# Kernel optimization log

Measured on AMD Instinct MI355X. Metric: run time of the kernel, lower is better.

## Reference

```python
import jax, jax.numpy as jnp
import numpy as np

EPSILON = 1e-4  # self.epsilon


def setup_inputs() -> dict:
    key = jax.random.key(0)
    ks = jax.random.split(key, 7)
    N, C_in, L = 32, 128, 512
    C_p, P, n_cls = 64, 2000, 200
    x = jax.random.normal(ks[0], (N, C_in, L), dtype=jnp.float32)
    W1 = jax.random.normal(ks[1], (C_p, C_in, 1), dtype=jnp.float32) * 0.05
    b1 = jnp.zeros((C_p,), dtype=jnp.float32)
    W2 = jax.random.normal(ks[2], (C_p, C_p, 1), dtype=jnp.float32) * 0.05
    b2 = jnp.zeros((C_p,), dtype=jnp.float32)
    prototype_vectors = jax.random.uniform(ks[3], (P, C_p, 1), dtype=jnp.float32)
    last_w = jax.random.normal(ks[4], (n_cls, P), dtype=jnp.float32) * 0.02
    return {"x": x, "W1": W1, "b1": b1, "W2": W2, "b2": b2,
            "prototype_vectors": prototype_vectors, "last_w": last_w}


def _forward(x, W1, b1, W2, b2, prototype_vectors, last_w):
    # add_on_layers: 1x1 conv1d -> relu -> 1x1 conv1d -> sigmoid
    h = jax.nn.relu(jnp.einsum('ncl,oc->nol', x, W1[:, :, 0]) + b1[None, :, None])
    f = jax.nn.sigmoid(jnp.einsum('ncl,oc->nol', h, W2[:, :, 0]) + b2[None, :, None])
    # _l2_convolution (prototype kernel length 1, stride 1):
    # x2_patch_sum via conv with all-ones filter == per-position channel sum of f^2
    x2_patch_sum = jnp.sum(f * f, axis=1, keepdims=True)          # [N,1,L]
    p2 = jnp.sum(prototype_vectors ** 2, axis=(1, 2))             # [P]
    xp = jnp.einsum('ncl,pc->npl', f, prototype_vectors[:, :, 0])  # [N,P,L]
    distances = jax.nn.relu(x2_patch_sum - 2.0 * xp + p2[None, :, None])
    # -max_pool(-d) over full length == min over L
    min_distances = jnp.min(distances, axis=2)                    # [N,P]
    prototype_activations = jnp.log((min_distances + 1.0) / (min_distances + EPSILON))
    logits = prototype_activations @ last_w.T                     # [N,num_classes]
    return logits, min_distances


def reference(x, W1, b1, W2, b2, prototype_vectors, last_w):
    return _forward(x, W1, b1, W2, b2, prototype_vectors, last_w)
```

## Files before the change

### kernel.cpp

```cpp
#include <hip/hip_runtime.h>
#include <hip/hip_fp16.h>
#include <math.h>

#define EPS 1e-4f
#define N_   32
#define CIN  128
#define L_   512
#define CP   64
#define P_   2000
#define NCLS 200

typedef __attribute__((ext_vector_type(8))) _Float16 f16x8;
typedef __attribute__((ext_vector_type(4))) float f32x4;

__device__ inline void gl_lds16(const void* g, void* l) {
    __builtin_amdgcn_global_load_lds(
        (const __attribute__((address_space(1))) unsigned int*)g,
        (__attribute__((address_space(3))) unsigned int*)l, 16, 0, 0);
}
__device__ inline unsigned int packh2(float a, float b) {
    unsigned int lo = __half_as_ushort(__float2half(a));
    unsigned int hi = __half_as_ushort(__float2half(b));
    return lo | (hi << 16);
}
__device__ inline unsigned short f2bf_rne(float f) {
    unsigned int u = __float_as_uint(f);
    unsigned int r = u + 0x7FFFu + ((u >> 16) & 1u);
    return (unsigned short)(r >> 16);
}
__device__ inline float bfdot2(unsigned a, unsigned b, float acc) {
    float a0 = __uint_as_float(a << 16);
    float a1 = __uint_as_float(a & 0xFFFF0000u);
    float b0 = __uint_as_float(b << 16);
    float b1 = __uint_as_float(b & 0xFFFF0000u);
    return fmaf(a1, b1, fmaf(a0, b0, acc));
}

__global__ __launch_bounds__(256) void k0_proto(const float* __restrict__ proto,
    const float* __restrict__ W1, const float* __restrict__ W2,
    const float* __restrict__ last_w,
    unsigned short* __restrict__ ph, unsigned short* __restrict__ w1h,
    unsigned short* __restrict__ w2h, unsigned short* __restrict__ lwB,
    float* __restrict__ p2)
{
    const int tid = threadIdx.x;
    const int bx  = blockIdx.x;
    if (bx >= 502) {
        int idx8 = (bx - 502)*256 + tid;
        if (idx8 < 50000) {
            const float4* src = (const float4*)(last_w + (size_t)idx8*8);
            float4 v0 = src[0], v1 = src[1];
            unsigned short o[8] = { f2bf_rne(v0.x), f2bf_rne(v0.y), f2bf_rne(v0.z), f2bf_rne(v0.w),
                                    f2bf_rne(v1.x), f2bf_rne(v1.y), f2bf_rne(v1.z), f2bf_rne(v1.w) };
            *(uint4*)(lwB + (size_t)idx8*8) = *(const uint4*)o;
        }
        return;
    }
    if (bx == 500) {
        #pragma unroll
        for (int i = 0; i < 32; ++i) {
            int idx = i*256 + tid;
            w1h[idx] = __half_as_ushort(__float2half(W1[idx]));
        }
        return;
    }
    if (bx == 501) {
        #pragma unroll
        for (int i = 0; i < 16; ++i) {
            int idx = i*256 + tid;
            w2h[idx] = __half_as_ushort(__float2half(W2[idx]));
        }
        return;
    }
    const int p = bx*4 + (tid >> 6);
    const int k = tid & 63;
    float v = proto[(size_t)p*64 + k];
    ph[(size_t)p*64 + k] = __half_as_ushort(__float2half(v));
    float s = v*v;
    #pragma unroll
    for (int off = 32; off > 0; off >>= 1) s += __shfl_xor(s, off);
    if (k == 0) p2[p] = s;
}

__global__ __launch_bounds__(256) void k1_conv(const float* __restrict__ x,
    const unsigned short* __restrict__ w1h, const float* __restrict__ b1,
    const unsigned short* __restrict__ w2h, const float* __restrict__ b2,
    unsigned short* __restrict__ fT, float* __restrict__ x2buf)
{
    __shared__ float xS[128*32];
    __shared__ __align__(16) unsigned short hb[32*72];
    __shared__ float x2p[2][32];

    const int tid  = threadIdx.x;
    const int lane = tid & 63;
    const int wv   = tid >> 6;
    const int n    = blockIdx.y;
    const int lg   = blockIdx.x;

    {
        const float* xbase = x + (size_t)n*CIN*L_ + lg*32;
        #pragma unroll
        for (int i = 0; i < 4; ++i) {
            int blk = wv*4 + i;
            const float* src = xbase + (size_t)(blk*8 + (lane >> 3))*L_ + (lane & 7)*4;
            gl_lds16(src, &xS[blk*256]);
        }
    }
    __syncthreads();

    const int r  = lane & 15;
    const int g  = lane >> 4;
    const int lt = wv & 1;
    const int oh = wv >> 1;
    const int lrow = lt*16 + r;

    f32x4 acc[2];
    #pragma unroll
    for (int o2 = 0; o2 < 2; ++o2)
        acc[o2] = *(const f32x4*)(b1 + (oh*2 + o2)*16 + g*4);

    #pragma unroll
    for (int ks = 0; ks < 4; ++ks) {
        f16x8 B;
        #pragma unroll
        for (int i = 0; i < 8; ++i)
            B[i] = (_Float16)xS[(ks*32 + g*8 + i)*32 + lrow];
        #pragma unroll
        for (int o2 = 0; o2 < 2; ++o2) {
            int ot = oh*2 + o2;
            f16x8 A = *(const f16x8*)(w1h + (ot*16 + r)*128 + ks*32 + g*8);
            acc[o2] = __builtin_amdgcn_mfma_f32_16x16x32_f16(A, B, acc[o2], 0, 0, 0);
        }
    }
    #pragma unroll
    for (int o2 = 0; o2 < 2; ++o2) {
        int ot = oh*2 + o2;
        float v0 = fmaxf(acc[o2][0], 0.f), v1 = fmaxf(acc[o2][1], 0.f);
        float v2 = fmaxf(acc[o2][2], 0.f), v3 = fmaxf(acc[o2][3], 0.f);
        uint2 w2v = make_uint2(packh2(v0, v1), packh2(v2, v3));
        *(uint2*)((char*)hb + lrow*144 + ot*32 + g*8) = w2v;
    }
    __syncthreads();

    f32x4 acc2[2];
    #pragma unroll
    for (int o2 = 0; o2 < 2; ++o2)
        acc2[o2] = *(const f32x4*)(b2 + (oh*2 + o2)*16 + g*4);

    #pragma unroll
    for (int ks = 0; ks < 2; ++ks) {
        f16x8 B = *(const f16x8*)((const char*)hb + lrow*144 + ks*64 + g*16);
        #pragma unroll
        for (int o2 = 0; o2 < 2; ++o2) {
            int ot = oh*2 + o2;
            f16x8 A = *(const f16x8*)(w2h + (ot*16 + r)*64 + ks*32 + g*8);
            acc2[o2] = __builtin_amdgcn_mfma_f32_16x16x32_f16(A, B, acc2[o2], 0, 0, 0);
        }
    }

    char* gb = (char*)xS;
    float s = 0.f;
    float fv[2][4];
    #pragma unroll
    for (int o2 = 0; o2 < 2; ++o2)
        #pragma unroll
        for (int j = 0; j < 4; ++j) {
            float v = 1.f/(1.f + expf(-acc2[o2][j]));
            fv[o2][j] = v;
            s = fmaf(v, v, s);
        }
    s += __shfl_xor(s, 16);
    s += __shfl_xor(s, 32);
    if (lane < 16) x2p[oh][lrow] = s;

    #pragma unroll
    for (int o2 = 0; o2 < 2; ++o2) {
        int ot = oh*2 + o2;
        uint2 w2v = make_uint2(packh2(fv[o2][0], fv[o2][1]), packh2(fv[o2][2], fv[o2][3]));
        *(uint2*)(gb + lrow*144 + ot*32 + g*8) = w2v;
    }
    __syncthreads();

    {
        int l = tid >> 3, u = tid & 7;
        uint4 v = *(const uint4*)(gb + l*144 + u*16);
        ((uint4*)fT)[((size_t)(n*L_ + lg*32 + l))*8 + u] = v;
    }
    if (tid < 32)
        x2buf[n*L_ + lg*32 + tid] = x2p[0][tid] + x2p[1][tid];
}

__global__ __launch_bounds__(256) void k2_dist(
    const unsigned short* __restrict__ fT, const unsigned short* __restrict__ ph,
    const float* __restrict__ x2buf, float* __restrict__ md_part)
{
    __shared__ unsigned short fB[4096];
    __shared__ float x2S[64];

    const int tid  = threadIdx.x;
    const int lane = tid & 63;
    const int wv   = tid >> 6;
    const int n    = blockIdx.y;
    const int lg   = blockIdx.x >> 2;
    const int pg   = blockIdx.x & 3;

    {
        const char* gH = (const char*)(fT + ((size_t)n*L_ + lg*64)*CP);
        #pragma unroll
        for (int j = 0; j < 2; ++j) {
            int d  = tid*32 + j*16;
            int lr = d >> 7;
            int bo = d & 127;
            int pb = (lr << 7) + (bo ^ ((lr & 7) << 4));
            *(uint4*)((char*)fB + pb) = *(const uint4*)(gH + d);
        }
    }
    if (tid < 64) x2S[tid] = x2buf[n*L_ + lg*64 + tid];
    __syncthreads();

    const int g  = lane >> 4;
    const int pr = lane & 15;

    f16x8 af[4][2];
    #pragma unroll
    for (int lt = 0; lt < 4; ++lt) {
        int lrow = lt*16 + pr;
        #pragma unroll
        for (int ks = 0; ks < 2; ++ks) {
            int bo = (ks*64 + g*16) ^ ((lrow & 7) << 4);
            af[lt][ks] = *(const f16x8*)((const char*)fB + lrow*128 + bo);
        }
    }
    float4 xv[4];
    #pragma unroll
    for (int lt = 0; lt < 4; ++lt)
        xv[lt] = *(const float4*)&x2S[lt*16 + g*4];

    float* mp = md_part + ((size_t)lg*N_ + n)*P_;

    const int t0 = pg + 4*wv;
    f16x8 bA[2], bB[2], bC[2];
    {
        const int p = t0*16 + pr;
        #pragma unroll
        for (int ks = 0; ks < 2; ++ks)
            bA[ks] = *(const f16x8*)(ph + (size_t)p*64 + ks*32 + g*8);
    }
    if (t0 + 16 < P_/16) {
        const int p = (t0+16)*16 + pr;
        #pragma unroll
        for (int ks = 0; ks < 2; ++ks)
            bB[ks] = *(const f16x8*)(ph + (size_t)p*64 + ks*32 + g*8);
    }
    for (int t = t0; t < P_/16; t += 16) {
        const int t2 = t + 32;
        if (t2 < P_/16) {
            const int p = t2*16 + pr;
            #pragma unroll
            for (int ks = 0; ks < 2; ++ks)
                bC[ks] = *(const f16x8*)(ph + (size_t)p*64 + ks*32 + g*8);
        }

        float cm0 = 3.0e38f, cm1 = 3.0e38f, cm2 = 3.0e38f, cm3 = 3.0e38f;
        #pragma unroll
        for (int lt = 0; lt < 4; ++lt) {
            f32x4 c = {0.f, 0.f, 0.f, 0.f};
            c = __builtin_amdgcn_mfma_f32_16x16x32_f16(af[lt][0], bA[0], c, 0, 0, 0);
            c = __builtin_amdgcn_mfma_f32_16x16x32_f16(af[lt][1], bA[1], c, 0, 0, 0);
            cm0 = fminf(cm0, fmaf(-2.f, c[0], xv[lt].x));
            cm1 = fminf(cm1, fmaf(-2.f, c[1], xv[lt].y));
            cm2 = fminf(cm2, fmaf(-2.f, c[2], xv[lt].z));
            cm3 = fminf(cm3, fmaf(-2.f, c[3], xv[lt].w));
        }
        float v = fminf(fminf(cm0, cm1), fminf(cm2, cm3));
        v = fminf(v, __shfl_xor(v, 16));
        v = fminf(v, __shfl_xor(v, 32));
        if (lane < 16) mp[t*16 + lane] = v;

        bA[0] = bB[0]; bA[1] = bB[1];
        bB[0] = bC[0]; bB[1] = bC[1];
    }
}

__global__ __launch_bounds__(256) void k2b_reduce(const float* __restrict__ md_part,
    const float* __restrict__ p2, float* __restrict__ md_out,
    unsigned short* __restrict__ actsB)
{
    const int p = blockIdx.x*256 + threadIdx.x;
    const int n = blockIdx.y;
    if (p < P_) {
        float mv = 3.0e38f;
        #pragma unroll
        for (int lg = 0; lg < 8; ++lg)
            mv = fminf(mv, md_part[((size_t)lg*N_ + n)*P_ + p]);
        float m = fmaxf(mv + p2[p], 0.0f);
        md_out[n*P_ + p] = m;
        actsB[(size_t)n*P_ + p] = f2bf_rne(logf((m + 1.0f) / (m + EPS)));
    }
}

__global__ __launch_bounds__(256) void k3_logits(const unsigned short* __restrict__ actsB,
    const unsigned short* __restrict__ lwB, float* __restrict__ out)
{
    const int wid  = (blockIdx.x * 256 + threadIdx.x) >> 6;
    const int lane = threadIdx.x & 63;
    const int n    = wid / NCLS;
    const int cls  = wid - n * NCLS;

    const uint4* a = (const uint4*)(actsB + (size_t)n*P_);
    const uint4* w = (const uint4*)(lwB + (size_t)cls*P_);

    float acc = 0.f;
    #pragma unroll
    for (int it = 0; it < 4; ++it) {
        int idx = it*64 + lane;
        if (idx < P_/8) {
            uint4 av = a[idx], wv = w[idx];
            acc = bfdot2(av.x, wv.x, acc);
            acc = bfdot2(av.y, wv.y, acc);
            acc = bfdot2(av.z, wv.z, acc);
            acc = bfdot2(av.w, wv.w, acc);
        }
    }
    #pragma unroll
    for (int off = 32; off > 0; off >>= 1)
        acc += __shfl_down(acc, off);
    if (lane == 0)
        out[n*NCLS + cls] = acc;
}

extern "C" void kernel_launch(void* const* d_in, const int* in_sizes, int n_in,
                              void* d_out, int out_size, void* d_ws, size_t ws_size,
                              hipStream_t stream)
{
    const float* x      = (const float*)d_in[0];
    const float* W1     = (const float*)d_in[1];
    const float* b1     = (const float*)d_in[2];
    const float* W2     = (const float*)d_in[3];
    const float* b2     = (const float*)d_in[4];
    const float* proto  = (const float*)d_in[5];
    const float* last_w = (const float*)d_in[6];

    float* out = (float*)d_out;

    unsigned short* fT = (unsigned short*)d_ws;
    float* x2buf = (float*)(fT + (size_t)N_*L_*CP);
    unsigned short* actsB = (unsigned short*)(x2buf + (size_t)N_*L_);
    unsigned short* ph = actsB + (size_t)N_*P_;
    float* p2      = (float*)(ph + (size_t)P_*CP);
    float* md_part = p2 + P_;
    unsigned short* w1h = (unsigned short*)(md_part + (size_t)8*N_*P_);
    unsigned short* w2h = w1h + 64*CIN;
    unsigned short* lwB = w2h + 64*CP;

    k0_proto  <<<698,           256, 0, stream>>>(proto, W1, W2, last_w,
                                                  ph, w1h, w2h, lwB, p2);
    k1_conv   <<<dim3(16, 32),  256, 0, stream>>>(x, w1h, b1, w2h, b2, fT, x2buf);
    k2_dist   <<<dim3(32, 32),  256, 0, stream>>>(fT, ph, x2buf, md_part);
    k2b_reduce<<<dim3(8, 32),   256, 0, stream>>>(md_part, p2, out + N_*NCLS, actsB);
    k3_logits <<<1600,          256, 0, stream>>>(actsB, lwB, out);
}
```

Before: 35.17 us.

## Fuse weight prep into conv kernel and reduce into logits kernel

Merges the prototype/weight conversion kernel into the conv kernel as extra blocks. W1/W2 are now converted to fp16 inline from fp32 global memory instead of through a separate precomputed buffer. Also fuses the min-reduction and activation computation with the logits GEMV, keeping activations in shared memory, so the launch count drops from five to three. In exchange, each of the 8 class-group blocks per sample recomputes the full reduction, and W1/W2 conversion work is repeated in every conv block.

```diff
diff --git a/kernel.cpp b/kernel.cpp
--- a/kernel.cpp
+++ b/kernel.cpp
@@ -35,67 +35,57 @@
     float b1 = __uint_as_float(b & 0xFFFF0000u);
     return fmaf(a1, b1, fmaf(a0, b0, acc));
 }
-
-__global__ __launch_bounds__(256) void k0_proto(const float* __restrict__ proto,
-    const float* __restrict__ W1, const float* __restrict__ W2,
-    const float* __restrict__ last_w,
-    unsigned short* __restrict__ ph, unsigned short* __restrict__ w1h,
-    unsigned short* __restrict__ w2h, unsigned short* __restrict__ lwB,
+__device__ inline f16x8 cvt8(const float* p) {
+    float4 a0 = *(const float4*)p, a1 = *(const float4*)(p + 4);
+    f16x8 r;
+    r[0]=(_Float16)a0.x; r[1]=(_Float16)a0.y; r[2]=(_Float16)a0.z; r[3]=(_Float16)a0.w;
+    r[4]=(_Float16)a1.x; r[5]=(_Float16)a1.y; r[6]=(_Float16)a1.z; r[7]=(_Float16)a1.w;
+    return r;
+}
+
+__global__ __launch_bounds__(256) void kA_conv_prep(const float* __restrict__ x,
+    const float* __restrict__ W1, const float* __restrict__ b1,
+    const float* __restrict__ W2, const float* __restrict__ b2,
+    const float* __restrict__ proto, const float* __restrict__ last_w,
+    unsigned short* __restrict__ fT, float* __restrict__ x2buf,
+    unsigned short* __restrict__ ph, unsigned short* __restrict__ lwB,
     float* __restrict__ p2)
-{
-    const int tid = threadIdx.x;
-    const int bx  = blockIdx.x;
-    if (bx >= 502) {
-        int idx8 = (bx - 502)*256 + tid;
-        if (idx8 < 50000) {
-            const float4* src = (const float4*)(last_w + (size_t)idx8*8);
-            float4 v0 = src[0], v1 = src[1];
-            unsigned short o[8] = { f2bf_rne(v0.x), f2bf_rne(v0.y), f2bf_rne(v0.z), f2bf_rne(v0.w),
-                                    f2bf_rne(v1.x), f2bf_rne(v1.y), f2bf_rne(v1.z), f2bf_rne(v1.w) };
-            *(uint4*)(lwB + (size_t)idx8*8) = *(const uint4*)o;
-        }
-        return;
-    }
-    if (bx == 500) {
-        #pragma unroll
-        for (int i = 0; i < 32; ++i) {
-            int idx = i*256 + tid;
-            w1h[idx] = __half_as_ushort(__float2half(W1[idx]));
-        }
-        return;
-    }
-    if (bx == 501) {
-        #pragma unroll
-        for (int i = 0; i < 16; ++i) {
-            int idx = i*256 + tid;
-            w2h[idx] = __half_as_ushort(__float2half(W2[idx]));
-        }
-        return;
-    }
-    const int p = bx*4 + (tid >> 6);
-    const int k = tid & 63;
-    float v = proto[(size_t)p*64 + k];
-    ph[(size_t)p*64 + k] = __half_as_ushort(__float2half(v));
-    float s = v*v;
-    #pragma unroll
-    for (int off = 32; off > 0; off >>= 1) s += __shfl_xor(s, off);
-    if (k == 0) p2[p] = s;
-}
-
-__global__ __launch_bounds__(256) void k1_conv(const float* __restrict__ x,
-    const unsigned short* __restrict__ w1h, const float* __restrict__ b1,
-    const unsigned short* __restrict__ w2h, const float* __restrict__ b2,
-    unsigned short* __restrict__ fT, float* __restrict__ x2buf)
 {
     __shared__ float xS[128*32];
     __shared__ __align__(16) unsigned short hb[32*72];
     __shared__ float x2p[2][32];
 
-    const int tid  = threadIdx.x;
+    const int tid = threadIdx.x;
+    const int bx  = blockIdx.x;
+
+    if (bx >= 512) {
+        const int pb = bx - 512;
+        if (pb < 500) {
+            const int p = pb*4 + (tid >> 6);
+            const int k = tid & 63;
+            float v = proto[(size_t)p*64 + k];
+            ph[(size_t)p*64 + k] = __half_as_ushort(__float2half(v));
+            float s = v*v;
+            #pragma unroll
+            for (int off = 32; off > 0; off >>= 1) s += __shfl_xor(s, off);
+            if (k == 0) p2[p] = s;
+        } else {
+            int idx8 = (pb - 500)*256 + tid;
+            if (idx8 < 50000) {
+                const float4* src = (const float4*)(last_w + (size_t)idx8*8);
+                float4 v0 = src[0], v1 = src[1];
+                unsigned short o[8] = { f2bf_rne(v0.x), f2bf_rne(v0.y), f2bf_rne(v0.z), f2bf_rne(v0.w),
+                                        f2bf_rne(v1.x), f2bf_rne(v1.y), f2bf_rne(v1.z), f2bf_rne(v1.w) };
+                *(uint4*)(lwB + (size_t)idx8*8) = *(const uint4*)o;
+            }
+        }
+        return;
+    }
+
     const int lane = tid & 63;
     const int wv   = tid >> 6;
-    const int n    = blockIdx.y;
-    const int lg   = blockIdx.x;
+    const int n    = bx >> 4;
+    const int lg   = bx & 15;
 
     {
         const float* xbase = x + (size_t)n*CIN*L_ + lg*32;
@@ -128,7 +118,7 @@
         #pragma unroll
         for (int o2 = 0; o2 < 2; ++o2) {
             int ot = oh*2 + o2;
-            f16x8 A = *(const f16x8*)(w1h + (ot*16 + r)*128 + ks*32 + g*8);
+            f16x8 A = cvt8(W1 + (size_t)(ot*16 + r)*128 + ks*32 + g*8);
             acc[o2] = __builtin_amdgcn_mfma_f32_16x16x32_f16(A, B, acc[o2], 0, 0, 0);
         }
     }
@@ -153,7 +143,7 @@
         #pragma unroll
         for (int o2 = 0; o2 < 2; ++o2) {
             int ot = oh*2 + o2;
-            f16x8 A = *(const f16x8*)(w2h + (ot*16 + r)*64 + ks*32 + g*8);
+            f16x8 A = cvt8(W2 + (size_t)(ot*16 + r)*64 + ks*32 + g*8);
             acc2[o2] = __builtin_amdgcn_mfma_f32_16x16x32_f16(A, B, acc2[o2], 0, 0, 0);
         }
     }
@@ -282,51 +272,62 @@
     }
 }
 
-__global__ __launch_bounds__(256) void k2b_reduce(const float* __restrict__ md_part,
-    const float* __restrict__ p2, float* __restrict__ md_out,
-    unsigned short* __restrict__ actsB)
+__global__ __launch_bounds__(256) void kC_reduce_logits(const float* __restrict__ md_part,
+    const float* __restrict__ p2, const unsigned short* __restrict__ lwB,
+    float* __restrict__ md_out, float* __restrict__ out)
 {
-    const int p = blockIdx.x*256 + threadIdx.x;
-    const int n = blockIdx.y;
-    if (p < P_) {
-        float mv = 3.0e38f;
-        #pragma unroll
-        for (int lg = 0; lg < 8; ++lg)
-            mv = fminf(mv, md_part[((size_t)lg*N_ + n)*P_ + p]);
-        float m = fmaxf(mv + p2[p], 0.0f);
-        md_out[n*P_ + p] = m;
-        actsB[(size_t)n*P_ + p] = f2bf_rne(logf((m + 1.0f) / (m + EPS)));
-    }
-}
-
-__global__ __launch_bounds__(256) void k3_logits(const unsigned short* __restrict__ actsB,
-    const unsigned short* __restrict__ lwB, float* __restrict__ out)
-{
-    const int wid  = (blockIdx.x * 256 + threadIdx.x) >> 6;
-    const int lane = threadIdx.x & 63;
-    const int n    = wid / NCLS;
-    const int cls  = wid - n * NCLS;
-
-    const uint4* a = (const uint4*)(actsB + (size_t)n*P_);
-    const uint4* w = (const uint4*)(lwB + (size_t)cls*P_);
-
-    float acc = 0.f;
+    __shared__ unsigned short actsS[2048];
+
+    const int tid  = threadIdx.x;
+    const int lane = tid & 63;
+    const int wv   = tid >> 6;
+    const int cg   = blockIdx.x;
+    const int n    = blockIdx.y;
+
+    #pragma unroll
+    for (int j = 0; j < 8; ++j) {
+        int p = j*256 + tid;
+        if (p < P_) {
+            float mv = 3.0e38f;
+            #pragma unroll
+            for (int lg = 0; lg < 8; ++lg)
+                mv = fminf(mv, md_part[((size_t)lg*N_ + n)*P_ + p]);
+            float m = fmaxf(mv + p2[p], 0.0f);
+            if (cg == 0) md_out[n*P_ + p] = m;
+            actsS[p] = f2bf_rne(logf((m + 1.0f) / (m + EPS)));
+        }
+    }
+    __syncthreads();
+
+    const uint4* a4 = (const uint4*)actsS;
+    uint4 av[4];
     #pragma unroll
     for (int it = 0; it < 4; ++it) {
-        int idx = it*64 + lane;
-        if (idx < P_/8) {
-            uint4 av = a[idx], wv = w[idx];
-            acc = bfdot2(av.x, wv.x, acc);
-            acc = bfdot2(av.y, wv.y, acc);
-            acc = bfdot2(av.z, wv.z, acc);
-            acc = bfdot2(av.w, wv.w, acc);
-        }
-    }
-    #pragma unroll
-    for (int off = 32; off > 0; off >>= 1)
-        acc += __shfl_down(acc, off);
-    if (lane == 0)
-        out[n*NCLS + cls] = acc;
+        int idx8 = it*64 + lane;
+        av[it] = (idx8 < 250) ? a4[idx8] : make_uint4(0,0,0,0);
+    }
+
+    for (int c = wv; c < 25; c += 4) {
+        const int cls = cg*25 + c;
+        const uint4* w4 = (const uint4*)(lwB + (size_t)cls*P_);
+        float acc = 0.f;
+        #pragma unroll
+        for (int it = 0; it < 4; ++it) {
+            int idx8 = it*64 + lane;
+            if (idx8 < 250) {
+                uint4 wv4 = w4[idx8];
+                acc = bfdot2(av[it].x, wv4.x, acc);
+                acc = bfdot2(av[it].y, wv4.y, acc);
+                acc = bfdot2(av[it].z, wv4.z, acc);
+                acc = bfdot2(av[it].w, wv4.w, acc);
+            }
+        }
+        #pragma unroll
+        for (int off = 32; off > 0; off >>= 1)
+            acc += __shfl_down(acc, off);
+        if (lane == 0)
+            out[n*NCLS + cls] = acc;
+    }
 }
 
 extern "C" void kernel_launch(void* const* d_in, const int* in_sizes, int n_in,
@@ -345,18 +346,14 @@
 
     unsigned short* fT = (unsigned short*)d_ws;
     float* x2buf = (float*)(fT + (size_t)N_*L_*CP);
-    unsigned short* actsB = (unsigned short*)(x2buf + (size_t)N_*L_);
-    unsigned short* ph = actsB + (size_t)N_*P_;
+    unsigned short* ph = (unsigned short*)(x2buf + (size_t)N_*L_);
     float* p2      = (float*)(ph + (size_t)P_*CP);
     float* md_part = p2 + P_;
-    unsigned short* w1h = (unsigned short*)(md_part + (size_t)8*N_*P_);
-    unsigned short* w2h = w1h + 64*CIN;
-    unsigned short* lwB = w2h + 64*CP;
-
-    k0_proto  <<<698,           256, 0, stream>>>(proto, W1, W2, last_w,
-                                                  ph, w1h, w2h, lwB, p2);
-    k1_conv   <<<dim3(16, 32),  256, 0, stream>>>(x, w1h, b1, w2h, b2, fT, x2buf);
-    k2_dist   <<<dim3(32, 32),  256, 0, stream>>>(fT, ph, x2buf, md_part);
-    k2b_reduce<<<dim3(8, 32),   256, 0, stream>>>(md_part, p2, out + N_*NCLS, actsB);
-    k3_logits <<<1600,          256, 0, stream>>>(actsB, lwB, out);
-}
+    unsigned short* lwB = (unsigned short*)(md_part + (size_t)8*N_*P_);
+
+    kA_conv_prep    <<<1208,          256, 0, stream>>>(x, W1, b1, W2, b2, proto, last_w,
+                                                        fT, x2buf, ph, lwB, p2);
+    k2_dist         <<<dim3(32, 32),  256, 0, stream>>>(fT, ph, x2buf, md_part);
+    kC_reduce_logits<<<dim3(8, 32),   256, 0, stream>>>(md_part, p2, lwB,
+                                                        out + N_*NCLS, out);
+}
```

Result: slower. 41.62 us (+18.4%).
